# Optimization experiments

Hardware: AMD Instinct MI355X
Metric: run time of the kernel (lower is better)

Reference implementation:

```python
import jax, jax.numpy as jnp
import numpy as np

NUM_HEADS = 16
D_MODEL = 1024
HEAD_DIM = D_MODEL // NUM_HEADS
EPS = 1e-6


def setup_inputs() -> dict:
    key = jax.random.key(0)
    ks = jax.random.split(key, 9)
    B, S, D = 4, 8192, D_MODEL
    scale = 1.0 / np.sqrt(D)  # variance_scaling(1.0, fan_in, normal) approx
    inputs_q = jax.random.normal(ks[0], (B, S, D), dtype=jnp.float32)
    Wq = jax.random.normal(ks[1], (D, D), dtype=jnp.float32) * scale
    Wk = jax.random.normal(ks[2], (D, D), dtype=jnp.float32) * scale
    Wv = jax.random.normal(ks[3], (D, D), dtype=jnp.float32) * scale
    Wo = jax.random.normal(ks[4], (D, D), dtype=jnp.float32) * scale
    bq = jnp.zeros((D,), jnp.float32)
    bk = jnp.zeros((D,), jnp.float32)
    bv = jnp.zeros((D,), jnp.float32)
    bo = jnp.zeros((D,), jnp.float32)
    return {"inputs_q": inputs_q, "Wq": Wq, "bq": bq, "Wk": Wk, "bk": bk,
            "Wv": Wv, "bv": bv, "Wo": Wo, "bo": bo}


def _feature_map(x):
    return jax.nn.elu(x) + 1.0


def reference(inputs_q, Wq, bq, Wk, bk, Wv, bv, Wo, bo):
    B, S, D = inputs_q.shape
    H, Dh = NUM_HEADS, HEAD_DIM
    # QKV projections (self-attention: k,v inputs default to q input)
    q = (inputs_q @ Wq + bq).reshape(B, S, H, Dh)
    k = (inputs_q @ Wk + bk).reshape(B, S, H, Dh)
    v = (inputs_q @ Wv + bv).reshape(B, S, H, Dh)
    q = _feature_map(q)
    k = _feature_map(k)
    # KV outer-product accumulation: [B, H, Dh, Dh]
    kv = jnp.einsum('bkhd,bkhm->bhdm', k, v)
    out = jnp.einsum('bqhd,bhdm->bqhm', q, kv)
    # normalizer: q . sum_k(k)
    normalizer = jnp.einsum('bqhd,bkhd->bqh', q, k)
    normalizer = jnp.maximum(normalizer, EPS)
    out = out / normalizer[..., None]
    out = out.reshape(B, S, D)
    return out @ Wo + bo
```

## Files before the change

### kernel.cpp

```cpp
#include <hip/hip_runtime.h>
#include <cstdint>
#include <cstddef>

#define D_MODEL 1024
#define SEQ 8192

typedef __bf16  bf16x8 __attribute__((ext_vector_type(8)));
typedef short   short8 __attribute__((ext_vector_type(8)));
typedef float   f32x4  __attribute__((ext_vector_type(4)));
typedef unsigned short ushort_t;

__device__ __forceinline__ ushort_t f2bf(float f) {
  uint32_t u = __builtin_bit_cast(uint32_t, f);
  u += 0x7FFFu + ((u >> 16) & 1u);
  return (ushort_t)(u >> 16);
}
__device__ __forceinline__ void gll16(const void* g, void* l) {
  __builtin_amdgcn_global_load_lds(
      (const __attribute__((address_space(1))) void*)g,
      (__attribute__((address_space(3))) void*)l, 16, 0, 0);
}
__device__ __forceinline__ void stage_half(const ushort_t* g, char* l0) {
  gll16(g, l0);
  gll16(g + 65536, l0 + 8192);
}

__global__ void k_convert_x(const float* __restrict__ x, ushort_t* __restrict__ xb, int n) {
  int i = (blockIdx.x * 256 + threadIdx.x) * 8;
  if (i >= n) return;
  float4 v0 = *(const float4*)(x + i);
  float4 v1 = *(const float4*)(x + i + 4);
  ushort_t o[8] = { f2bf(v0.x), f2bf(v0.y), f2bf(v0.z), f2bf(v0.w),
                    f2bf(v1.x), f2bf(v1.y), f2bf(v1.z), f2bf(v1.w) };
  *(short8*)(xb + i) = *(const short8*)o;
}

__global__ void k_transpose_w(const float* W0, const float* W1, const float* W2, const float* W3,
                              ushort_t* Tqkv, ushort_t* To) {
  const float* src; ushort_t* dst;
  switch (blockIdx.z) {
    case 0: src = W0; dst = Tqkv; break;
    case 1: src = W1; dst = Tqkv + (size_t)1024 * 1024; break;
    case 2: src = W2; dst = Tqkv + (size_t)2048 * 1024; break;
    default: src = W3; dst = To; break;
  }
  __shared__ float tile[64][65];
  int tx = threadIdx.x;
  int c = tx & 63, r0 = tx >> 6;
  int bx = blockIdx.x * 64, by = blockIdx.y * 64;
  #pragma unroll
  for (int i = 0; i < 16; i++) {
    int r = i * 4 + r0;
    tile[r][c] = src[(size_t)(by + r) * D_MODEL + bx + c];
  }
  __syncthreads();
  #pragma unroll
  for (int i = 0; i < 16; i++) {
    int r = i * 4 + r0;
    dst[(size_t)(bx + r) * D_MODEL + by + c] = f2bf(tile[c][r]);
  }
}

template<int MODE, int NY>
__global__ __launch_bounds__(512, 2) void k_gemm(const ushort_t* __restrict__ A,
                                                 const ushort_t* __restrict__ Bt,
                                                 const float* __restrict__ b0,
                                                 const float* __restrict__ b1,
                                                 const float* __restrict__ b2,
                                                 ushort_t* __restrict__ o0,
                                                 ushort_t* __restrict__ o1,
                                                 ushort_t* __restrict__ o2,
                                                 float* __restrict__ outf) {
  __shared__ __align__(16) char smem[131072];

  const int nwg = gridDim.x;
  const int bid0 = blockIdx.x;
  const int bid = (bid0 & 7) * (nwg >> 3) + (bid0 >> 3);
  const int xb = bid / NY, yb = bid % NY;
  const int m0 = xb * 256, n0 = yb * 256;

  const int tid = threadIdx.x;
  const int ln = tid & 63;
  const int w  = tid >> 6;
  const int wb = __builtin_amdgcn_readfirstlane(w);
  const int wm = wb >> 2, wn = wb & 3;

  const int srow = wb * 8 + (ln >> 3);
  const int schk = ((ln & 7) ^ ((ln >> 3) & 7)) * 8;
  const ushort_t* gA = A  + (size_t)(m0 + srow) * D_MODEL + schk;
  const ushort_t* gB = Bt + (size_t)(n0 + srow) * D_MODEL + schk;

#define STG_A(BASE, H, T) stage_half(gA + (size_t)(T) * 64 + (size_t)(H) * 131072, smem + (BASE) + (H) * 16384 + wb * 1024)
#define STG_B(BASE, H, T) stage_half(gB + (size_t)(T) * 64 + (size_t)(H) * 131072, smem + (BASE) + 32768 + (H) * 16384 + wb * 1024)

#define VMW_(N) asm volatile("s_waitcnt vmcnt(" #N ")" ::: "memory")
#define VMW(N)  VMW_(N)
#define LGW_(N) asm volatile("s_waitcnt lgkmcnt(" #N ")" ::: "memory")
#define LGW__(N) LGW_(N)
#define LGW(N)  do { LGW__(N); __builtin_amdgcn_sched_barrier(0); } while (0)

  f32x4 acc[8][4];
  #pragma unroll
  for (int i = 0; i < 8; i++)
    #pragma unroll
    for (int j = 0; j < 4; j++) acc[i][j] = (f32x4){0.f, 0.f, 0.f, 0.f};
  bf16x8 aX[2][2], aY[2][2];
  bf16x8 bX[4][2], bY[4][2];

  const int ar  = ln & 15;
  const int cw0 = (((ln >> 4)    ) ^ (ln & 7)) << 4;
  const int cw1 = (((ln >> 4) + 4) ^ (ln & 7)) << 4;
  const int arow = wm * 128 + ar;
  const int brow = wn * 64 + ar;

#define LDA2(DST, BASE, CH) { _Pragma("unroll") for (int m_ = 0; m_ < 2; ++m_) { \
    const char* p_ = smem + (BASE) + ((arow + (CH) * 32 + m_ * 16) << 7); \
    DST[m_][0] = *(const bf16x8*)(p_ + cw0); DST[m_][1] = *(const bf16x8*)(p_ + cw1); } }
#define LDB2(DST, BASE, J0) { _Pragma("unroll") for (int j_ = 0; j_ < 2; ++j_) { \
    const char* p_ = smem + (BASE) + 32768 + ((brow + ((J0) + j_) * 16) << 7); \
    DST[(J0) + j_][0] = *(const bf16x8*)(p_ + cw0); DST[(J0) + j_][1] = *(const bf16x8*)(p_ + cw1); } }
#define MF8(P, ASET, BSET) { _Pragma("unroll") for (int m_ = 0; m_ < 2; ++m_) \
    _Pragma("unroll") for (int j_ = 0; j_ < 4; ++j_) { \
      acc[(P)*2+m_][j_] = __builtin_amdgcn_mfma_f32_16x16x32_bf16(ASET[m_][0], BSET[j_][0], acc[(P)*2+m_][j_], 0, 0, 0); \
      acc[(P)*2+m_][j_] = __builtin_amdgcn_mfma_f32_16x16x32_bf16(ASET[m_][1], BSET[j_][1], acc[(P)*2+m_][j_], 0, 0, 0); } }

#define BARSB { __builtin_amdgcn_s_barrier(); __builtin_amdgcn_sched_barrier(0); }

#define TILE(T, CUR, NXT, BC, BN, H1, H2, LA, LB, LC, V1) { \
     \
    if (H1) STG_A(NXT, 0, (T) + 1); \
    LDA2(aY, CUR, 1); \
    LGW(4); \
    __builtin_amdgcn_s_setprio(1); MF8(0, aX, BC); __builtin_amdgcn_s_setprio(0); \
    if (H1) VMW(2);                   \
    BARSB; \
     \
    if (H1) STG_A(NXT, 1, (T) + 1); \
    LDA2(aX, CUR, 2); \
    if (H1) LDB2(BN, NXT, 0); \
    LGW(LA); \
    __builtin_amdgcn_s_setprio(1); MF8(1, aY, BC); __builtin_amdgcn_s_setprio(0); \
     \
    if (H2) STG_B(CUR, 0, (T) + 2); \
    LDA2(aY, CUR, 3); \
    if (H1) LDB2(BN, NXT, 2); \
    LGW(LB); \
    __builtin_amdgcn_s_setprio(1); MF8(2, aX, BC); __builtin_amdgcn_s_setprio(0); \
    if (H1) VMW(V1);                  \
    BARSB; \
     \
    if (H2) STG_B(CUR, 1, (T) + 2); \
    if (H1) LDA2(aX, NXT, 0); \
    LGW(LC); \
    __builtin_amdgcn_s_setprio(1); MF8(3, aY, BC); __builtin_amdgcn_s_setprio(0); \
    BARSB; \
  }

  STG_A(0, 0, 0); STG_A(0, 1, 0); STG_B(0, 0, 0); STG_B(0, 1, 0);
  STG_B(65536, 0, 1); STG_B(65536, 1, 1);
  VMW(4);
  __builtin_amdgcn_s_barrier();
  __builtin_amdgcn_sched_barrier(0);
  LDA2(aX, 0, 0);
  LDB2(bX, 0, 0); LDB2(bX, 0, 2);

  #pragma unroll 1
  for (int kt = 0; kt < 14; kt += 2) {
    TILE(kt,     0,     65536, bX, bY, true, true, 8, 12, 8, 2);
    TILE(kt + 1, 65536, 0,     bY, bX, true, true, 8, 12, 8, 2);
  }
  TILE(14, 0,     65536, bX, bY, true,  false, 8, 12, 8, 0);
  TILE(15, 65536, 0,     bY, bX, false, false, 4, 4, 0, 2);

#undef STG_A
#undef STG_B
#undef LDA2
#undef LDB2
#undef MF8
#undef TILE
#undef BARSB

  const int colb = ln & 15, rowb = (ln >> 4) * 4;

  if constexpr (MODE == 0) {
    const int region = yb >> 2;
    const int nl0 = (yb & 3) * 256;
    const float* bias = region == 0 ? b0 : (region == 1 ? b1 : b2);
    ushort_t* gout    = region == 0 ? o0 : (region == 1 ? o1 : o2);
    const bool act = region < 2;
    ushort_t* Cs = (ushort_t*)smem;
    #pragma unroll
    for (int j = 0; j < 4; ++j) {
      const int col = wn * 64 + j * 16 + colb;
      const float bv_ = bias[nl0 + col];
      #pragma unroll
      for (int i = 0; i < 8; ++i) {
        const int rb_ = wm * 128 + i * 16 + rowb;
        #pragma unroll
        for (int r = 0; r < 4; ++r) {
          float v = acc[i][j][r] + bv_;
          if (act) v = (v > 0.f) ? v + 1.f : __expf(v);
          const int row = rb_ + r;
          const int ch = col >> 3;
          Cs[row * 256 + ((ch ^ (row & 31)) << 3) + (col & 7)] = f2bf(v);
        }
      }
    }
    __syncthreads();
    #pragma unroll
    for (int c = 0; c < 16; ++c) {
      const int idx = c * 512 + tid;
      const int row = idx >> 5, ch = idx & 31;
      short8 t = *(const short8*)&Cs[row * 256 + ((ch ^ (row & 31)) << 3)];
      *(short8*)&gout[(size_t)(m0 + row) * D_MODEL + nl0 + ch * 8] = t;
    }
  } else {
    float* Cf = (float*)smem;
    #pragma unroll
    for (int h = 0; h < 2; ++h) {
      if (h) __syncthreads();
      if (wm == h) {
        #pragma unroll
        for (int j = 0; j < 4; ++j) {
          const int col = wn * 64 + j * 16 + colb;
          const float bv_ = b0[n0 + col];
          #pragma unroll
          for (int i = 0; i < 8; ++i) {
            const int rl = i * 16 + rowb;
            #pragma unroll
            for (int r = 0; r < 4; ++r) {
              const int row = rl + r;
              const int ch = col >> 2;
              Cf[row * 256 + ((ch ^ (row & 7)) << 2) + (col & 3)] = acc[i][j][r] + bv_;
            }
          }
        }
      }
      __syncthreads();
      #pragma unroll
      for (int c = 0; c < 16; ++c) {
        const int idx = c * 512 + tid;
        const int row = idx >> 6, ch = idx & 63;
        float4 t = *(const float4*)&Cf[row * 256 + ((ch ^ (row & 7)) << 2)];
        *(float4*)&outf[(size_t)(m0 + h * 128 + row) * D_MODEL + n0 + ch * 4] = t;
      }
    }
  }
#undef VMW_
#undef VMW
#undef LGW_
#undef LGW__
#undef LGW
}

__global__ __launch_bounds__(256) void k_kv_partial(const ushort_t* __restrict__ kmat,
                                                    const ushort_t* __restrict__ vmat,
                                                    float* __restrict__ part) {
  __shared__ __align__(16) ushort_t sbuf[4][2][2][512];
  const int tid = threadIdx.x, ln = tid & 63, w = tid >> 6;
  const int wb = __builtin_amdgcn_readfirstlane(w);
  const int bh = blockIdx.y, chunk = blockIdx.x;
  const int b = bh >> 4, h = bh & 15;
  const size_t cbase = ((size_t)b * SEQ + chunk * 1024 + w * 256) * D_MODEL + h * 64;
  const ushort_t* gk = kmat + cbase + (size_t)(ln >> 3) * D_MODEL + (ln & 7) * 8;
  const ushort_t* gv = vmat + cbase + (size_t)(ln >> 3) * D_MODEL + (ln & 7) * 8;

  float acc[8][8];
  float ksum[8];
  #pragma unroll
  for (int i = 0; i < 8; i++) { ksum[i] = 0.f;
    #pragma unroll
    for (int j = 0; j < 8; j++) acc[i][j] = 0.f; }

  const int r8 = (ln >> 3) * 8, c8 = (ln & 7) * 8;
  gll16(gk, &sbuf[wb][0][0][0]);
  gll16(gv, &sbuf[wb][0][1][0]);
  gk += 8 * D_MODEL; gv += 8 * D_MODEL;

  for (int bt = 0; bt < 32; bt++) {
    const int p = bt & 1;
    if (bt < 31) {
      gll16(gk, &sbuf[wb][p ^ 1][0][0]);
      gll16(gv, &sbuf[wb][p ^ 1][1][0]);
      gk += 8 * D_MODEL; gv += 8 * D_MODEL;
      __builtin_amdgcn_s_waitcnt(0x0F72);
    } else {
      __builtin_amdgcn_s_waitcnt(0x0F70);
    }
    #pragma unroll
    for (int s = 0; s < 8; s++) {
      short8 kk = *(const short8*)&sbuf[wb][p][0][s * 64 + r8];
      short8 vv = *(const short8*)&sbuf[wb][p][1][s * 64 + c8];
      float ka[8], va[8];
      #pragma unroll
      for (int i = 0; i < 8; i++) {
        ka[i] = __builtin_bit_cast(float, (uint32_t)(ushort_t)kk[i] << 16);
        va[i] = __builtin_bit_cast(float, (uint32_t)(ushort_t)vv[i] << 16);
      }
      #pragma unroll
      for (int i = 0; i < 8; i++) {
        ksum[i] += ka[i];
        #pragma unroll
        for (int j = 0; j < 8; j++) acc[i][j] += ka[i] * va[j];
      }
    }
  }
  float* p0 = part + ((size_t)bh * 32 + chunk * 4 + w) * 4160;
  #pragma unroll
  for (int i = 0; i < 8; i++)
    #pragma unroll
    for (int j = 0; j < 8; j++) p0[(r8 + i) * 64 + c8 + j] = acc[i][j];
  if ((ln & 7) == 0) {
    #pragma unroll
    for (int i = 0; i < 8; i++) p0[4096 + r8 + i] = ksum[i];
  }
}

__global__ void k_kv_reduce(const float* __restrict__ part, ushort_t* __restrict__ kvt) {
  const int bh = blockIdx.x, tid = threadIdx.x;
  const float* p0 = part + (size_t)bh * 32 * 4160;
  for (int idx = tid; idx < 4160; idx += 256) {
    float s = 0.f;
    #pragma unroll 4
    for (int c = 0; c < 32; c++) s += p0[(size_t)c * 4160 + idx];
    ushort_t bf = f2bf(s);
    if (idx < 4096) { int d = idx >> 6, m = idx & 63; kvt[(size_t)bh * 4160 + m * 64 + d] = bf; }
    else            { kvt[(size_t)bh * 4160 + 4096 + (idx - 4096)] = bf; }
  }
}

__global__ __launch_bounds__(256) void k_attn(const ushort_t* __restrict__ qmat,
                                              const ushort_t* __restrict__ kvt,
                                              ushort_t* __restrict__ attn) {
  __shared__ __align__(16) ushort_t kvs[65 * 80];
  __shared__ __align__(16) ushort_t qs[4][64 * 80];
  const int tid = threadIdx.x, ln = tid & 63, w = tid >> 6;
  const int bh = blockIdx.y, b = bh >> 4, h = bh & 15;

  for (int idx = tid; idx < 4160; idx += 256) {
    int m = idx >> 6, d = idx & 63;
    kvs[m * 80 + d] = kvt[(size_t)bh * 4160 + idx];
  }
  const size_t s0 = (size_t)b * SEQ + blockIdx.x * 256 + w * 64;
  #pragma unroll
  for (int c = 0; c < 8; c++) {
    int f = c * 64 + ln;
    int row = f >> 3, dg = (f & 7) * 8;
    short8 t = *(const short8*)&qmat[(s0 + row) * D_MODEL + h * 64 + dg];
    *(short8*)&qs[w][row * 80 + dg] = t;
  }
  __syncthreads();

  const int ar = ln & 15, aq = (ln >> 4) * 8;
  f32x4 acc[4][4], nacc[4];
  #pragma unroll
  for (int i = 0; i < 4; i++) { nacc[i] = (f32x4){0.f, 0.f, 0.f, 0.f};
    #pragma unroll
    for (int j = 0; j < 4; j++) acc[i][j] = (f32x4){0.f, 0.f, 0.f, 0.f}; }

  #pragma unroll
  for (int kk = 0; kk < 2; kk++) {
    const int ko = kk * 32 + aq;
    bf16x8 a[4], bb[4], bn;
    #pragma unroll
    for (int i = 0; i < 4; i++) a[i] = *(const bf16x8*)&qs[w][(i * 16 + ar) * 80 + ko];
    #pragma unroll
    for (int j = 0; j < 4; j++) bb[j] = *(const bf16x8*)&kvs[(j * 16 + ar) * 80 + ko];
    bn = *(const bf16x8*)&kvs[64 * 80 + ko];
    #pragma unroll
    for (int i = 0; i < 4; i++) {
      #pragma unroll
      for (int j = 0; j < 4; j++)
        acc[i][j] = __builtin_amdgcn_mfma_f32_16x16x32_bf16(a[i], bb[j], acc[i][j], 0, 0, 0);
      nacc[i] = __builtin_amdgcn_mfma_f32_16x16x32_bf16(a[i], bn, nacc[i], 0, 0, 0);
    }
  }

  const int colb = ln & 15, rowb = (ln >> 4) * 4;
  #pragma unroll
  for (int i = 0; i < 4; i++) {
    #pragma unroll
    for (int r = 0; r < 4; r++) {
      const int row = i * 16 + rowb + r;
      float nm = fmaxf(nacc[i][r], 1e-6f);
      float inv = 1.0f / nm;
      const size_t grow = s0 + row;
      #pragma unroll
      for (int j = 0; j < 4; j++) {
        float v = acc[i][j][r] * inv;
        attn[grow * D_MODEL + h * 64 + j * 16 + colb] = f2bf(v);
      }
    }
  }
}

extern "C" void kernel_launch(void* const* d_in, const int* in_sizes, int n_in,
                              void* d_out, int out_size, void* d_ws, size_t ws_size,
                              hipStream_t stream) {
  const float* x  = (const float*)d_in[0];
  const float* Wq = (const float*)d_in[1];
  const float* bq = (const float*)d_in[2];
  const float* Wk = (const float*)d_in[3];
  const float* bk = (const float*)d_in[4];
  const float* Wv = (const float*)d_in[5];
  const float* bv = (const float*)d_in[6];
  const float* Wo = (const float*)d_in[7];
  const float* bo = (const float*)d_in[8];
  float* out = (float*)d_out;

  const int M = in_sizes[0] / D_MODEL;
  const int B = M / SEQ;
  const int BH = B * 16;

  char* ws = (char*)d_ws;
  size_t off = 0;
  auto alloc = [&](size_t bytes) { char* p = ws + off; off += (bytes + 255) & ~(size_t)255; return p; };
  const size_t mb = (size_t)M * D_MODEL * 2;
  ushort_t* xb    = (ushort_t*)alloc(mb);
  ushort_t* qb    = (ushort_t*)alloc(mb);
  ushort_t* kb    = (ushort_t*)alloc(mb);
  ushort_t* vb    = (ushort_t*)alloc(mb);
  ushort_t* attnb = (ushort_t*)alloc(mb);
  ushort_t* wqkvt = (ushort_t*)alloc((size_t)3 * D_MODEL * D_MODEL * 2);
  ushort_t* wot   = (ushort_t*)alloc((size_t)D_MODEL * D_MODEL * 2);
  ushort_t* kvt   = (ushort_t*)alloc((size_t)BH * 4160 * 2);
  float*    part  = (float*)   alloc((size_t)BH * 32 * 4160 * 4);
  (void)ws_size; (void)n_in; (void)out_size;

  const int n = M * D_MODEL;
  k_convert_x<<<n / (256 * 8), 256, 0, stream>>>(x, xb, n);
  k_transpose_w<<<dim3(16, 16, 4), 256, 0, stream>>>(Wq, Wk, Wv, Wo, wqkvt, wot);

  k_gemm<0, 12><<<(M / 256) * 12, 512, 0, stream>>>(xb, wqkvt, bq, bk, bv, qb, kb, vb, nullptr);

  k_kv_partial<<<dim3(8, BH), 256, 0, stream>>>(kb, vb, part);
  k_kv_reduce<<<BH, 256, 0, stream>>>(part, kvt);
  k_attn<<<dim3(SEQ / 256, BH), 256, 0, stream>>>(qb, kvt, attnb);

  k_gemm<2, 4><<<(M / 256) * 4, 512, 0, stream>>>(attnb, wot, bo, nullptr, nullptr, nullptr, nullptr, nullptr, out);
}
```

Before: 673.8 us.

## Restructure GEMM main loop into quadrant-based MFMA schedule with reordered staging

Reorganizes the bf16 GEMM inner loop to split each K-tile's 256x256 output into four quadrants (two A halves by two B halves). A and B fragments are loaded per half, and global-to-LDS staging of the next tiles is interleaved with the quadrant MFMA phases under a different prefetch order and wait counts. The aim is better overlap of LDS reads, global loads and MFMA work while reusing register fragments across quadrants. It adds more barriers per tile (eight instead of three), which could cost synchronization time.

```diff
diff --git a/kernel.cpp b/kernel.cpp
--- a/kernel.cpp
+++ b/kernel.cpp
@@ -98,87 +98,83 @@
 #define LGW_(N) asm volatile("s_waitcnt lgkmcnt(" #N ")" ::: "memory")
 #define LGW__(N) LGW_(N)
 #define LGW(N)  do { LGW__(N); __builtin_amdgcn_sched_barrier(0); } while (0)
+#define BARSB { __builtin_amdgcn_s_barrier(); __builtin_amdgcn_sched_barrier(0); }
 
   f32x4 acc[8][4];
   #pragma unroll
   for (int i = 0; i < 8; i++)
     #pragma unroll
     for (int j = 0; j < 4; j++) acc[i][j] = (f32x4){0.f, 0.f, 0.f, 0.f};
-  bf16x8 aX[2][2], aY[2][2];
-  bf16x8 bX[4][2], bY[4][2];
+  bf16x8 a0f[4][2], a1f[4][2];
+  bf16x8 b0f[2][2], b1f[2][2];
 
   const int ar  = ln & 15;
   const int cw0 = (((ln >> 4)    ) ^ (ln & 7)) << 4;
   const int cw1 = (((ln >> 4) + 4) ^ (ln & 7)) << 4;
-  const int arow = wm * 128 + ar;
-  const int brow = wn * 64 + ar;
-
-#define LDA2(DST, BASE, CH) { _Pragma("unroll") for (int m_ = 0; m_ < 2; ++m_) { \
-    const char* p_ = smem + (BASE) + ((arow + (CH) * 32 + m_ * 16) << 7); \
+
+#define LDAH(DST, BASE, MH) { _Pragma("unroll") for (int m_ = 0; m_ < 4; ++m_) { \
+    const char* p_ = smem + (BASE) + ((wm * 128 + (MH) * 64 + m_ * 16 + ar) << 7); \
     DST[m_][0] = *(const bf16x8*)(p_ + cw0); DST[m_][1] = *(const bf16x8*)(p_ + cw1); } }
-#define LDB2(DST, BASE, J0) { _Pragma("unroll") for (int j_ = 0; j_ < 2; ++j_) { \
-    const char* p_ = smem + (BASE) + 32768 + ((brow + ((J0) + j_) * 16) << 7); \
-    DST[(J0) + j_][0] = *(const bf16x8*)(p_ + cw0); DST[(J0) + j_][1] = *(const bf16x8*)(p_ + cw1); } }
-#define MF8(P, ASET, BSET) { _Pragma("unroll") for (int m_ = 0; m_ < 2; ++m_) \
-    _Pragma("unroll") for (int j_ = 0; j_ < 4; ++j_) { \
-      acc[(P)*2+m_][j_] = __builtin_amdgcn_mfma_f32_16x16x32_bf16(ASET[m_][0], BSET[j_][0], acc[(P)*2+m_][j_], 0, 0, 0); \
-      acc[(P)*2+m_][j_] = __builtin_amdgcn_mfma_f32_16x16x32_bf16(ASET[m_][1], BSET[j_][1], acc[(P)*2+m_][j_], 0, 0, 0); } }
-
-#define BARSB { __builtin_amdgcn_s_barrier(); __builtin_amdgcn_sched_barrier(0); }
-
-#define TILE(T, CUR, NXT, BC, BN, H1, H2, LA, LB, LC, V1) { \
+#define LDBH(DST, BASE, NH) { _Pragma("unroll") for (int j_ = 0; j_ < 2; ++j_) { \
+    const char* p_ = smem + (BASE) + 32768 + ((wn * 64 + (NH) * 32 + j_ * 16 + ar) << 7); \
+    DST[j_][0] = *(const bf16x8*)(p_ + cw0); DST[j_][1] = *(const bf16x8*)(p_ + cw1); } }
+#define QUAD(MH, NH, AF, BF) { _Pragma("unroll") for (int m_ = 0; m_ < 4; ++m_) \
+    _Pragma("unroll") for (int j_ = 0; j_ < 2; ++j_) { \
+      acc[(MH)*4+m_][(NH)*2+j_] = __builtin_amdgcn_mfma_f32_16x16x32_bf16(AF[m_][0], BF[j_][0], acc[(MH)*4+m_][(NH)*2+j_], 0, 0, 0); \
+      acc[(MH)*4+m_][(NH)*2+j_] = __builtin_amdgcn_mfma_f32_16x16x32_bf16(AF[m_][1], BF[j_][1], acc[(MH)*4+m_][(NH)*2+j_], 0, 0, 0); } }
+
+#define TILE(T, BT, BN, S1, S2, R1, LP2, LP3) { \
      \
-    if (H1) STG_A(NXT, 0, (T) + 1); \
-    LDA2(aY, CUR, 1); \
+    LDAH(a1f, BT, 1); \
+    if (S1) STG_B(BN, 1, (T) + 1); \
+    BARSB; \
+    LGW(8); \
+    __builtin_amdgcn_s_setprio(1); QUAD(0, 0, a0f, b0f); __builtin_amdgcn_s_setprio(0); \
+    BARSB; \
+     \
+    LDBH(b1f, BT, 1); \
+    BARSB; \
     LGW(4); \
-    __builtin_amdgcn_s_setprio(1); MF8(0, aX, BC); __builtin_amdgcn_s_setprio(0); \
-    if (H1) VMW(2);                   \
+    __builtin_amdgcn_s_setprio(1); QUAD(1, 0, a1f, b0f); __builtin_amdgcn_s_setprio(0); \
+    VMW(0); \
     BARSB; \
      \
-    if (H1) STG_A(NXT, 1, (T) + 1); \
-    LDA2(aX, CUR, 2); \
-    if (H1) LDB2(BN, NXT, 0); \
-    LGW(LA); \
-    __builtin_amdgcn_s_setprio(1); MF8(1, aY, BC); __builtin_amdgcn_s_setprio(0); \
+    if (R1) LDBH(b0f, BN, 0); \
+    if (S2) STG_A(BT, 0, (T) + 2); \
+    BARSB; \
+    LGW(LP2); \
+    __builtin_amdgcn_s_setprio(1); QUAD(0, 1, a0f, b1f); __builtin_amdgcn_s_setprio(0); \
+    BARSB; \
      \
-    if (H2) STG_B(CUR, 0, (T) + 2); \
-    LDA2(aY, CUR, 3); \
-    if (H1) LDB2(BN, NXT, 2); \
-    LGW(LB); \
-    __builtin_amdgcn_s_setprio(1); MF8(2, aX, BC); __builtin_amdgcn_s_setprio(0); \
-    if (H1) VMW(V1);                  \
-    BARSB; \
-     \
-    if (H2) STG_B(CUR, 1, (T) + 2); \
-    if (H1) LDA2(aX, NXT, 0); \
-    LGW(LC); \
-    __builtin_amdgcn_s_setprio(1); MF8(3, aY, BC); __builtin_amdgcn_s_setprio(0); \
+    if (R1) LDAH(a0f, BN, 0); \
+    if (S2) { STG_A(BT, 1, (T) + 2); STG_B(BT, 0, (T) + 2); } \
+    BARSB; \
+    LGW(LP3); \
+    __builtin_amdgcn_s_setprio(1); QUAD(1, 1, a1f, b1f); __builtin_amdgcn_s_setprio(0); \
     BARSB; \
   }
 
   STG_A(0, 0, 0); STG_A(0, 1, 0); STG_B(0, 0, 0); STG_B(0, 1, 0);
-  STG_B(65536, 0, 1); STG_B(65536, 1, 1);
-  VMW(4);
-  __builtin_amdgcn_s_barrier();
-  __builtin_amdgcn_sched_barrier(0);
-  LDA2(aX, 0, 0);
-  LDB2(bX, 0, 0); LDB2(bX, 0, 2);
+  STG_A(65536, 0, 1); STG_A(65536, 1, 1); STG_B(65536, 0, 1);
+  VMW(6);
+  BARSB;
+  LDAH(a0f, 0, 0);
+  LDBH(b0f, 0, 0);
 
   #pragma unroll 1
   for (int kt = 0; kt < 14; kt += 2) {
-    TILE(kt,     0,     65536, bX, bY, true, true, 8, 12, 8, 2);
-    TILE(kt + 1, 65536, 0,     bY, bX, true, true, 8, 12, 8, 2);
-  }
-  TILE(14, 0,     65536, bX, bY, true,  false, 8, 12, 8, 0);
-  TILE(15, 65536, 0,     bY, bX, false, false, 4, 4, 0, 2);
+    TILE(kt,     0,     65536, true, true, true, 4, 8);
+    TILE(kt + 1, 65536, 0,     true, true, true, 4, 8);
+  }
+  TILE(14, 0,     65536, true,  false, true,  4, 8);
+  TILE(15, 65536, 0,     false, false, false, 0, 0);
 
 #undef STG_A
 #undef STG_B
-#undef LDA2
-#undef LDB2
-#undef MF8
+#undef LDAH
+#undef LDBH
+#undef QUAD
 #undef TILE
-#undef BARSB
 
   const int colb = ln & 15, rowb = (ln >> 4) * 4;
 
@@ -251,6 +247,7 @@
 #undef LGW_
 #undef LGW__
 #undef LGW
+#undef BARSB
 }
 
 __global__ __launch_bounds__(256) void k_kv_partial(const ushort_t* __restrict__ kmat,
```

After: 807.9 us. +19.9%, slower.
